# Kernel tuning notes

Measured on AMD Instinct MI355X. Metric: run time of the kernel, lower is better.

## Reference

```python
import jax, jax.numpy as jnp
import numpy as np

# neighbor-sampled node counts per hop level (outermost -> batch)
SIZES = (1363968, 123904, 11264, 1024)
E = (1239040, 112640, 10240)
D_IN, D_H, D_OUT = 128, 256, 64


def _sage(x_src, x_dst, src, dst, Wl, bl, Wr):
    """PyG SAGEConv(aggr='mean') on bipartite (x_src, x_dst) graph."""
    n_dst = x_dst.shape[0]
    agg = jax.ops.segment_sum(x_src[src], dst, num_segments=n_dst)
    cnt = jax.ops.segment_sum(jnp.ones((src.shape[0],), x_src.dtype), dst, num_segments=n_dst)
    mean = agg / jnp.maximum(cnt, 1.0)[:, None]
    return mean @ Wl + bl + x_dst @ Wr  # lin_l(mean) + lin_r(x_dst), lin_r has no bias


def setup_inputs() -> dict:
    key = jax.random.key(0)
    ks = jax.random.split(key, 16)
    inp = {}
    inp["x"] = jax.random.normal(ks[0], (SIZES[0], D_IN), dtype=jnp.float32)
    dims = [(D_IN, D_H), (D_H, D_H), (D_H, D_OUT)]
    for i, (di, do) in enumerate(dims):
        s = 1.0 / np.sqrt(di)
        inp[f"Wl{i}"] = jax.random.uniform(ks[1 + 3 * i], (di, do), jnp.float32, -s, s)
        inp[f"bl{i}"] = jax.random.uniform(ks[2 + 3 * i], (do,), jnp.float32, -s, s)
        inp[f"Wr{i}"] = jax.random.uniform(ks[3 + 3 * i], (di, do), jnp.float32, -s, s)
    for i in range(3):
        inp[f"edge_src{i}"] = jax.random.randint(ks[10 + i * 2], (E[i],), 0, SIZES[i], dtype=jnp.int32)
        inp[f"edge_dst{i}"] = jax.random.randint(ks[11 + i * 2 - 1], (E[i],), 0, SIZES[i + 1], dtype=jnp.int32)
    return inp


def reference(x, Wl0, bl0, Wr0, Wl1, bl1, Wr1, Wl2, bl2, Wr2,
              edge_src0, edge_dst0, edge_src1, edge_dst1, edge_src2, edge_dst2):
    # layer 0 (i=0 != num_layers-1=1 -> relu; dropout is identity in eval)
    h = _sage(x, x[:SIZES[1]], edge_src0, edge_dst0, Wl0, bl0, Wr0)
    h = jax.nn.relu(h)
    # layer 1 (i=1 == num_layers-1 -> no relu)
    h = _sage(h, h[:SIZES[2]], edge_src1, edge_dst1, Wl1, bl1, Wr1)
    # layer 2 (i=2 != 1 -> relu, faithful to the original quirk)
    h = _sage(h, h[:SIZES[3]], edge_src2, edge_dst2, Wl2, bl2, Wr2)
    h = jax.nn.relu(h)
    return h
```

## Files before the change

kernel.cpp:

```cpp
#include <hip/hip_runtime.h>

#define SZ0 1363968
#define SZ1 123904
#define SZ2 11264
#define SZ3 1024
#define NE0 1239040
#define NE1 112640
#define NE2 10240
#define DIN 128
#define DH  256
#define DOUT 64

__global__ __launch_bounds__(256) void edge_hist(
    const int* __restrict__ dst, int* __restrict__ bk, int E)
{
    int e = blockIdx.x * 256 + threadIdx.x;
    if (e < E) atomicAdd(&bk[dst[e]], 1);
}

__global__ __launch_bounds__(1024) void scan_inplace(int* __restrict__ a, int n)
{
    __shared__ int sums[1024];
    const int t = threadIdx.x;
    const int C = (n + 1023) >> 10;
    const int lo = t * C;
    const int hi = min(lo + C, n);
    int s = 0;
    for (int i = lo; i < hi; i++) s += a[i];
    sums[t] = s;
    __syncthreads();
    for (int off = 1; off < 1024; off <<= 1) {
        int v = (t >= off) ? sums[t - off] : 0;
        __syncthreads();
        sums[t] += v;
        __syncthreads();
    }
    int pre = (t == 0) ? 0 : sums[t - 1];
    for (int i = lo; i < hi; i++) { int v = a[i]; a[i] = pre; pre += v; }
}

__global__ __launch_bounds__(256) void edge_bucket(
    const int* __restrict__ src, const int* __restrict__ dst,
    int* __restrict__ bk, int* __restrict__ perm, int E)
{
    int e = blockIdx.x * 256 + threadIdx.x;
    if (e < E) {
        int pos = atomicAdd(&bk[dst[e]], 1);
        perm[pos] = src[e];
    }
}

template <int D>
__global__ __launch_bounds__(256) void gather_mean(
    const float* __restrict__ X, const int* __restrict__ perm,
    const int* __restrict__ ends, float* __restrict__ out)
{
    constexpr int VEC = D / 64;
    const int wave = (blockIdx.x * 256 + threadIdx.x) >> 6;
    const int lane = threadIdx.x & 63;
    const int start = (wave == 0) ? 0 : ends[wave - 1];
    const int end = ends[wave];

    float acc0[VEC], acc1[VEC];
#pragma unroll
    for (int i = 0; i < VEC; i++) { acc0[i] = 0.0f; acc1[i] = 0.0f; }

    int e = start;
    for (; e + 2 <= end; e += 2) {
        int s0 = perm[e];
        int s1 = perm[e + 1];
        const float* p0 = X + (size_t)s0 * D + lane * VEC;
        const float* p1 = X + (size_t)s1 * D + lane * VEC;
        if (VEC == 2) {
            float2 v0 = *reinterpret_cast<const float2*>(p0);
            float2 v1 = *reinterpret_cast<const float2*>(p1);
            acc0[0] += v0.x; acc0[1] += v0.y;
            acc1[0] += v1.x; acc1[1] += v1.y;
        } else {
            float4 v0 = *reinterpret_cast<const float4*>(p0);
            float4 v1 = *reinterpret_cast<const float4*>(p1);
            acc0[0] += v0.x; acc0[1] += v0.y; acc0[2] += v0.z; acc0[3] += v0.w;
            acc1[0] += v1.x; acc1[1] += v1.y; acc1[2] += v1.z; acc1[3] += v1.w;
        }
    }
    if (e < end) {
        int s0 = perm[e];
        const float* p0 = X + (size_t)s0 * D + lane * VEC;
        if (VEC == 2) {
            float2 v0 = *reinterpret_cast<const float2*>(p0);
            acc0[0] += v0.x; acc0[1] += v0.y;
        } else {
            float4 v0 = *reinterpret_cast<const float4*>(p0);
            acc0[0] += v0.x; acc0[1] += v0.y; acc0[2] += v0.z; acc0[3] += v0.w;
        }
    }

    const float inv = 1.0f / (float)max(end - start, 1);
    float* o = out + (size_t)wave * D + lane * VEC;
    if (VEC == 2) {
        float2 v;
        v.x = (acc0[0] + acc1[0]) * inv;
        v.y = (acc0[1] + acc1[1]) * inv;
        *reinterpret_cast<float2*>(o) = v;
    } else {
        float4 v;
        v.x = (acc0[0] + acc1[0]) * inv;
        v.y = (acc0[1] + acc1[1]) * inv;
        v.z = (acc0[2] + acc1[2]) * inv;
        v.w = (acc0[3] + acc1[3]) * inv;
        *reinterpret_cast<float4*>(o) = v;
    }
}

template <int BM, int BN>
__global__ __launch_bounds__(256) void gemm_sage(
    const float* __restrict__ A1, const float* __restrict__ A2,
    const float* __restrict__ B1, const float* __restrict__ B2,
    const float* __restrict__ bias, float* __restrict__ C,
    int K1, int K2, int do_relu)
{
    constexpr int BK = 32;
    constexpr int ROWS = BM / 16;
    constexpr int G = BN / 64;
    constexpr int AF4 = (BM * 8) / 256;
    constexpr int BF4 = (BN * 8) / 256;

    __shared__ float As[BK][BM + 4];
    __shared__ float Bs[BK][BN + 4];

    const int tid = threadIdx.x;
    const int m0 = blockIdx.x * BM;
    const int ty = tid >> 4;
    const int tx = tid & 15;

    float acc[ROWS][G * 4];
#pragma unroll
    for (int i = 0; i < ROWS; i++)
#pragma unroll
        for (int j = 0; j < G * 4; j++) acc[i][j] = 0.0f;

    const int K = K1 + K2;
    for (int kt = 0; kt < K; kt += BK) {
        const float* Ap; const float* Bp; int lK, kof;
        if (kt < K1) { Ap = A1; Bp = B1; lK = K1; kof = kt; }
        else         { Ap = A2; Bp = B2; lK = K2; kof = kt - K1; }

#pragma unroll
        for (int j = 0; j < AF4; j++) {
            int id = tid * AF4 + j;
            int m = id >> 3;
            int q = id & 7;
            float4 v = *reinterpret_cast<const float4*>(
                Ap + (size_t)(m0 + m) * lK + kof + q * 4);
            As[q * 4 + 0][m] = v.x;
            As[q * 4 + 1][m] = v.y;
            As[q * 4 + 2][m] = v.z;
            As[q * 4 + 3][m] = v.w;
        }
#pragma unroll
        for (int j = 0; j < BF4; j++) {
            int id = tid * BF4 + j;
            int k = id / (BN / 4);
            int c = id % (BN / 4);
            float4 v = *reinterpret_cast<const float4*>(
                Bp + (size_t)(kof + k) * BN + c * 4);
            *reinterpret_cast<float4*>(&Bs[k][c * 4]) = v;
        }
        __syncthreads();

#pragma unroll
        for (int kk = 0; kk < BK; kk++) {
            float a[ROWS];
            if constexpr (ROWS == 4) {
                float4 av = *reinterpret_cast<const float4*>(&As[kk][ty * 4]);
                a[0] = av.x; a[1] = av.y; a[2] = av.z; a[3] = av.w;
            } else {
                float2 av = *reinterpret_cast<const float2*>(&As[kk][ty * 2]);
                a[0] = av.x; a[1] = av.y;
            }
#pragma unroll
            for (int g = 0; g < G; g++) {
                float4 bv = *reinterpret_cast<const float4*>(&Bs[kk][g * 64 + tx * 4]);
                const float b[4] = {bv.x, bv.y, bv.z, bv.w};
#pragma unroll
                for (int i = 0; i < ROWS; i++)
#pragma unroll
                    for (int jj = 0; jj < 4; jj++)
                        acc[i][g * 4 + jj] += a[i] * b[jj];
            }
        }
        __syncthreads();
    }

#pragma unroll
    for (int i = 0; i < ROWS; i++) {
        const int row = m0 + ty * ROWS + i;
#pragma unroll
        for (int g = 0; g < G; g++) {
            const float4 bb = *reinterpret_cast<const float4*>(bias + g * 64 + tx * 4);
            float v0 = acc[i][g * 4 + 0] + bb.x;
            float v1 = acc[i][g * 4 + 1] + bb.y;
            float v2 = acc[i][g * 4 + 2] + bb.z;
            float v3 = acc[i][g * 4 + 3] + bb.w;
            if (do_relu) {
                v0 = fmaxf(v0, 0.0f); v1 = fmaxf(v1, 0.0f);
                v2 = fmaxf(v2, 0.0f); v3 = fmaxf(v3, 0.0f);
            }
            float4 o; o.x = v0; o.y = v1; o.z = v2; o.w = v3;
            *reinterpret_cast<float4*>(C + (size_t)row * BN + g * 64 + tx * 4) = o;
        }
    }
}

extern "C" void kernel_launch(void* const* d_in, const int* in_sizes, int n_in,
                              void* d_out, int out_size, void* d_ws, size_t ws_size,
                              hipStream_t stream)
{
    const float* x   = (const float*)d_in[0];
    const float* Wl0 = (const float*)d_in[1];
    const float* bl0 = (const float*)d_in[2];
    const float* Wr0 = (const float*)d_in[3];
    const float* Wl1 = (const float*)d_in[4];
    const float* bl1 = (const float*)d_in[5];
    const float* Wr1 = (const float*)d_in[6];
    const float* Wl2 = (const float*)d_in[7];
    const float* bl2 = (const float*)d_in[8];
    const float* Wr2 = (const float*)d_in[9];
    const int* es0 = (const int*)d_in[10];
    const int* ed0 = (const int*)d_in[11];
    const int* es1 = (const int*)d_in[12];
    const int* ed1 = (const int*)d_in[13];
    const int* es2 = (const int*)d_in[14];
    const int* ed2 = (const int*)d_in[15];

    int* bk0   = (int*)d_ws;
    int* bk1   = bk0 + SZ1;
    int* bk2   = bk1 + SZ2;
    int* perm0 = bk2 + SZ3;
    int* perm1 = perm0 + NE0;
    int* perm2 = perm1 + NE1;
    float* agg0 = (float*)(perm2 + NE2);
    float* agg1 = agg0 + (size_t)SZ1 * DIN;
    float* agg2 = agg1 + (size_t)SZ2 * DH;
    float* h1   = agg2 + (size_t)SZ3 * DH;
    float* h2   = agg0;

    hipMemsetAsync(bk0, 0, (size_t)(SZ1 + SZ2 + SZ3) * sizeof(int), stream);

    edge_hist<<<(NE0 + 255) / 256, 256, 0, stream>>>(ed0, bk0, NE0);
    scan_inplace<<<1, 1024, 0, stream>>>(bk0, SZ1);
    edge_bucket<<<(NE0 + 255) / 256, 256, 0, stream>>>(es0, ed0, bk0, perm0, NE0);
    gather_mean<DIN><<<SZ1 / 4, 256, 0, stream>>>(x, perm0, bk0, agg0);
    gemm_sage<64, DH><<<SZ1 / 64, 256, 0, stream>>>(
        agg0, x, Wl0, Wr0, bl0, h1, DIN, DIN, 1);

    edge_hist<<<(NE1 + 255) / 256, 256, 0, stream>>>(ed1, bk1, NE1);
    scan_inplace<<<1, 1024, 0, stream>>>(bk1, SZ2);
    edge_bucket<<<(NE1 + 255) / 256, 256, 0, stream>>>(es1, ed1, bk1, perm1, NE1);
    gather_mean<DH><<<SZ2 / 4, 256, 0, stream>>>(h1, perm1, bk1, agg1);
    gemm_sage<32, DH><<<SZ2 / 32, 256, 0, stream>>>(
        agg1, h1, Wl1, Wr1, bl1, h2, DH, DH, 0);

    edge_hist<<<(NE2 + 255) / 256, 256, 0, stream>>>(ed2, bk2, NE2);
    scan_inplace<<<1, 1024, 0, stream>>>(bk2, SZ3);
    edge_bucket<<<(NE2 + 255) / 256, 256, 0, stream>>>(es2, ed2, bk2, perm2, NE2);
    gather_mean<DH><<<SZ3 / 4, 256, 0, stream>>>(h2, perm2, bk2, agg2);
    gemm_sage<32, DOUT><<<SZ3 / 32, 256, 0, stream>>>(
        agg2, h2, Wl2, Wr2, bl2, (float*)d_out, DH, DH, 1);
}
```

Measured before the change: 1.643 ms.

## Fuse layer-0 gather-mean into GEMM and batch CSR build across layers

Layer 0's neighbor mean aggregation is now computed directly into shared memory inside a fused gather+GEMM kernel. This removes the round trip of the 123904x128 aggregate buffer through global memory and one launch. The histogram, scan and bucket passes for all three layers are merged into single launches, cutting nine small kernels to three and letting the three scans run in parallel blocks. The gather_mean kernel is specialized to float4 only, and h2 gets its own buffer instead of aliasing agg0.

```diff
diff --git a/kernel.cpp b/kernel.cpp
--- a/kernel.cpp
+++ b/kernel.cpp
@@ -11,16 +11,31 @@
 #define DH  256
 #define DOUT 64
 
-__global__ __launch_bounds__(256) void edge_hist(
-    const int* __restrict__ dst, int* __restrict__ bk, int E)
+__global__ __launch_bounds__(256) void hist_all(
+    const int* __restrict__ ed0, const int* __restrict__ ed1,
+    const int* __restrict__ ed2, int* __restrict__ bk0,
+    int* __restrict__ bk1, int* __restrict__ bk2)
 {
     int e = blockIdx.x * 256 + threadIdx.x;
-    if (e < E) atomicAdd(&bk[dst[e]], 1);
-}
-
-__global__ __launch_bounds__(1024) void scan_inplace(int* __restrict__ a, int n)
+    if (e < NE0) {
+        atomicAdd(&bk0[ed0[e]], 1);
+    } else if (e < NE0 + NE1) {
+        atomicAdd(&bk1[ed1[e - NE0]], 1);
+    } else {
+        atomicAdd(&bk2[ed2[e - NE0 - NE1]], 1);
+    }
+}
+
+__global__ __launch_bounds__(1024) void scan_all(
+    int* __restrict__ a0, int n0, int* __restrict__ a1, int n1,
+    int* __restrict__ a2, int n2)
 {
     __shared__ int sums[1024];
+    int* a; int n;
+    if (blockIdx.x == 0)      { a = a0; n = n0; }
+    else if (blockIdx.x == 1) { a = a1; n = n1; }
+    else                      { a = a2; n = n2; }
+
     const int t = threadIdx.x;
     const int C = (n + 1023) >> 10;
     const int lo = t * C;
@@ -39,14 +54,25 @@
     for (int i = lo; i < hi; i++) { int v = a[i]; a[i] = pre; pre += v; }
 }
 
-__global__ __launch_bounds__(256) void edge_bucket(
-    const int* __restrict__ src, const int* __restrict__ dst,
-    int* __restrict__ bk, int* __restrict__ perm, int E)
+__global__ __launch_bounds__(256) void bucket_all(
+    const int* __restrict__ es0, const int* __restrict__ ed0,
+    const int* __restrict__ es1, const int* __restrict__ ed1,
+    const int* __restrict__ es2, const int* __restrict__ ed2,
+    int* __restrict__ bk0, int* __restrict__ bk1, int* __restrict__ bk2,
+    int* __restrict__ p0, int* __restrict__ p1, int* __restrict__ p2)
 {
     int e = blockIdx.x * 256 + threadIdx.x;
-    if (e < E) {
-        int pos = atomicAdd(&bk[dst[e]], 1);
-        perm[pos] = src[e];
+    if (e < NE0) {
+        int pos = atomicAdd(&bk0[ed0[e]], 1);
+        p0[pos] = es0[e];
+    } else if (e < NE0 + NE1) {
+        int i = e - NE0;
+        int pos = atomicAdd(&bk1[ed1[i]], 1);
+        p1[pos] = es1[i];
+    } else {
+        int i = e - NE0 - NE1;
+        int pos = atomicAdd(&bk2[ed2[i]], 1);
+        p2[pos] = es2[i];
     }
 }
 
@@ -71,44 +97,140 @@
         int s1 = perm[e + 1];
         const float* p0 = X + (size_t)s0 * D + lane * VEC;
         const float* p1 = X + (size_t)s1 * D + lane * VEC;
-        if (VEC == 2) {
-            float2 v0 = *reinterpret_cast<const float2*>(p0);
-            float2 v1 = *reinterpret_cast<const float2*>(p1);
-            acc0[0] += v0.x; acc0[1] += v0.y;
-            acc1[0] += v1.x; acc1[1] += v1.y;
-        } else {
-            float4 v0 = *reinterpret_cast<const float4*>(p0);
-            float4 v1 = *reinterpret_cast<const float4*>(p1);
-            acc0[0] += v0.x; acc0[1] += v0.y; acc0[2] += v0.z; acc0[3] += v0.w;
-            acc1[0] += v1.x; acc1[1] += v1.y; acc1[2] += v1.z; acc1[3] += v1.w;
-        }
+        float4 v0 = *reinterpret_cast<const float4*>(p0);
+        float4 v1 = *reinterpret_cast<const float4*>(p1);
+        acc0[0] += v0.x; acc0[1] += v0.y; acc0[2] += v0.z; acc0[3] += v0.w;
+        acc1[0] += v1.x; acc1[1] += v1.y; acc1[2] += v1.z; acc1[3] += v1.w;
     }
     if (e < end) {
         int s0 = perm[e];
         const float* p0 = X + (size_t)s0 * D + lane * VEC;
-        if (VEC == 2) {
-            float2 v0 = *reinterpret_cast<const float2*>(p0);
-            acc0[0] += v0.x; acc0[1] += v0.y;
-        } else {
-            float4 v0 = *reinterpret_cast<const float4*>(p0);
-            acc0[0] += v0.x; acc0[1] += v0.y; acc0[2] += v0.z; acc0[3] += v0.w;
-        }
+        float4 v0 = *reinterpret_cast<const float4*>(p0);
+        acc0[0] += v0.x; acc0[1] += v0.y; acc0[2] += v0.z; acc0[3] += v0.w;
     }
 
     const float inv = 1.0f / (float)max(end - start, 1);
     float* o = out + (size_t)wave * D + lane * VEC;
-    if (VEC == 2) {
-        float2 v;
-        v.x = (acc0[0] + acc1[0]) * inv;
-        v.y = (acc0[1] + acc1[1]) * inv;
-        *reinterpret_cast<float2*>(o) = v;
-    } else {
-        float4 v;
-        v.x = (acc0[0] + acc1[0]) * inv;
-        v.y = (acc0[1] + acc1[1]) * inv;
-        v.z = (acc0[2] + acc1[2]) * inv;
-        v.w = (acc0[3] + acc1[3]) * inv;
-        *reinterpret_cast<float4*>(o) = v;
+    float4 v;
+    v.x = (acc0[0] + acc1[0]) * inv;
+    v.y = (acc0[1] + acc1[1]) * inv;
+    v.z = (acc0[2] + acc1[2]) * inv;
+    v.w = (acc0[3] + acc1[3]) * inv;
+    *reinterpret_cast<float4*>(o) = v;
+}
+
+__global__ __launch_bounds__(256) void fused_sage0(
+    const float* __restrict__ X, const int* __restrict__ perm,
+    const int* __restrict__ ends, const float* __restrict__ B1,
+    const float* __restrict__ B2, const float* __restrict__ bias,
+    float* __restrict__ C)
+{
+    __shared__ float Am[DIN][68];
+    __shared__ float Bs[32][260];
+
+    const int tid = threadIdx.x;
+    const int m0 = blockIdx.x * 64;
+    const int wv = tid >> 6;
+    const int lane = tid & 63;
+
+    for (int r = wv; r < 64; r += 4) {
+        const int row = m0 + r;
+        const int start = (row == 0) ? 0 : ends[row - 1];
+        const int end = ends[row];
+        float a0 = 0, a1 = 0, b0 = 0, b1 = 0, c0 = 0, c1 = 0, d0 = 0, d1 = 0;
+        int e = start;
+        for (; e + 4 <= end; e += 4) {
+            int s0 = perm[e], s1 = perm[e + 1], s2 = perm[e + 2], s3 = perm[e + 3];
+            float2 v0 = *(const float2*)(X + (size_t)s0 * DIN + lane * 2);
+            float2 v1 = *(const float2*)(X + (size_t)s1 * DIN + lane * 2);
+            float2 v2 = *(const float2*)(X + (size_t)s2 * DIN + lane * 2);
+            float2 v3 = *(const float2*)(X + (size_t)s3 * DIN + lane * 2);
+            a0 += v0.x; a1 += v0.y; b0 += v1.x; b1 += v1.y;
+            c0 += v2.x; c1 += v2.y; d0 += v3.x; d1 += v3.y;
+        }
+        for (; e < end; e++) {
+            int s0 = perm[e];
+            float2 v0 = *(const float2*)(X + (size_t)s0 * DIN + lane * 2);
+            a0 += v0.x; a1 += v0.y;
+        }
+        const float inv = 1.0f / (float)max(end - start, 1);
+        Am[lane * 2 + 0][r] = (a0 + b0 + c0 + d0) * inv;
+        Am[lane * 2 + 1][r] = (a1 + b1 + c1 + d1) * inv;
+    }
+    __syncthreads();
+
+    const int ty = tid >> 4;
+    const int tx = tid & 15;
+
+    float acc[4][16];
+#pragma unroll
+    for (int i = 0; i < 4; i++)
+#pragma unroll
+        for (int j = 0; j < 16; j++) acc[i][j] = 0.0f;
+
+    for (int kt = 0; kt < 2 * DIN; kt += 32) {
+        int abase;
+        if (kt < DIN) {
+            abase = kt;
+        } else {
+            abase = 0;
+#pragma unroll
+            for (int j = 0; j < 2; j++) {
+                int id = tid * 2 + j;
+                int m = id >> 3;
+                int q = id & 7;
+                float4 v = *reinterpret_cast<const float4*>(
+                    X + (size_t)(m0 + m) * DIN + (kt - DIN) + q * 4);
+                Am[q * 4 + 0][m] = v.x;
+                Am[q * 4 + 1][m] = v.y;
+                Am[q * 4 + 2][m] = v.z;
+                Am[q * 4 + 3][m] = v.w;
+            }
+        }
+        const float* Bp = (kt < DIN) ? B1 : B2;
+        const int kof = (kt < DIN) ? kt : kt - DIN;
+#pragma unroll
+        for (int j = 0; j < 8; j++) {
+            int id = tid * 8 + j;
+            int k = id >> 6;
+            int c = id & 63;
+            float4 v = *reinterpret_cast<const float4*>(
+                Bp + (size_t)(kof + k) * DH + c * 4);
+            *reinterpret_cast<float4*>(&Bs[k][c * 4]) = v;
+        }
+        __syncthreads();
+
+#pragma unroll
+        for (int kk = 0; kk < 32; kk++) {
+            float4 av = *reinterpret_cast<const float4*>(&Am[abase + kk][ty * 4]);
+            const float a[4] = {av.x, av.y, av.z, av.w};
+#pragma unroll
+            for (int g = 0; g < 4; g++) {
+                float4 bv = *reinterpret_cast<const float4*>(&Bs[kk][g * 64 + tx * 4]);
+                const float b[4] = {bv.x, bv.y, bv.z, bv.w};
+#pragma unroll
+                for (int i = 0; i < 4; i++)
+#pragma unroll
+                    for (int jj = 0; jj < 4; jj++)
+                        acc[i][g * 4 + jj] += a[i] * b[jj];
+            }
+        }
+        __syncthreads();
+    }
+
+#pragma unroll
+    for (int i = 0; i < 4; i++) {
+        const int row = m0 + ty * 4 + i;
+#pragma unroll
+        for (int g = 0; g < 4; g++) {
+            const float4 bb = *reinterpret_cast<const float4*>(bias + g * 64 + tx * 4);
+            float v0 = fmaxf(acc[i][g * 4 + 0] + bb.x, 0.0f);
+            float v1 = fmaxf(acc[i][g * 4 + 1] + bb.y, 0.0f);
+            float v2 = fmaxf(acc[i][g * 4 + 2] + bb.z, 0.0f);
+            float v3 = fmaxf(acc[i][g * 4 + 3] + bb.w, 0.0f);
+            float4 o; o.x = v0; o.y = v1; o.z = v2; o.w = v3;
+            *reinterpret_cast<float4*>(C + (size_t)row * DH + g * 64 + tx * 4) = o;
+        }
     }
 }
 
@@ -239,31 +361,25 @@
     int* perm0 = bk2 + SZ3;
     int* perm1 = perm0 + NE0;
     int* perm2 = perm1 + NE1;
-    float* agg0 = (float*)(perm2 + NE2);
-    float* agg1 = agg0 + (size_t)SZ1 * DIN;
+    float* agg1 = (float*)(perm2 + NE2);
     float* agg2 = agg1 + (size_t)SZ2 * DH;
     float* h1   = agg2 + (size_t)SZ3 * DH;
-    float* h2   = agg0;
+    float* h2   = h1 + (size_t)SZ1 * DH;
 
     hipMemsetAsync(bk0, 0, (size_t)(SZ1 + SZ2 + SZ3) * sizeof(int), stream);
 
-    edge_hist<<<(NE0 + 255) / 256, 256, 0, stream>>>(ed0, bk0, NE0);
-    scan_inplace<<<1, 1024, 0, stream>>>(bk0, SZ1);
-    edge_bucket<<<(NE0 + 255) / 256, 256, 0, stream>>>(es0, ed0, bk0, perm0, NE0);
-    gather_mean<DIN><<<SZ1 / 4, 256, 0, stream>>>(x, perm0, bk0, agg0);
-    gemm_sage<64, DH><<<SZ1 / 64, 256, 0, stream>>>(
-        agg0, x, Wl0, Wr0, bl0, h1, DIN, DIN, 1);
-
-    edge_hist<<<(NE1 + 255) / 256, 256, 0, stream>>>(ed1, bk1, NE1);
-    scan_inplace<<<1, 1024, 0, stream>>>(bk1, SZ2);
-    edge_bucket<<<(NE1 + 255) / 256, 256, 0, stream>>>(es1, ed1, bk1, perm1, NE1);
+    constexpr int NET = NE0 + NE1 + NE2;
+    hist_all<<<NET / 256, 256, 0, stream>>>(ed0, ed1, ed2, bk0, bk1, bk2);
+    scan_all<<<3, 1024, 0, stream>>>(bk0, SZ1, bk1, SZ2, bk2, SZ3);
+    bucket_all<<<NET / 256, 256, 0, stream>>>(es0, ed0, es1, ed1, es2, ed2,
+                                              bk0, bk1, bk2, perm0, perm1, perm2);
+
+    fused_sage0<<<SZ1 / 64, 256, 0, stream>>>(x, perm0, bk0, Wl0, Wr0, bl0, h1);
+
     gather_mean<DH><<<SZ2 / 4, 256, 0, stream>>>(h1, perm1, bk1, agg1);
     gemm_sage<32, DH><<<SZ2 / 32, 256, 0, stream>>>(
         agg1, h1, Wl1, Wr1, bl1, h2, DH, DH, 0);
 
-    edge_hist<<<(NE2 + 255) / 256, 256, 0, stream>>>(ed2, bk2, NE2);
-    scan_inplace<<<1, 1024, 0, stream>>>(bk2, SZ3);
-    edge_bucket<<<(NE2 + 255) / 256, 256, 0, stream>>>(es2, ed2, bk2, perm2, NE2);
     gather_mean<DH><<<SZ3 / 4, 256, 0, stream>>>(h2, perm2, bk2, agg2);
     gemm_sage<32, DOUT><<<SZ3 / 32, 256, 0, stream>>>(
         agg2, h2, Wl2, Wr2, bl2, (float*)d_out, DH, DH, 1);
```

Result: slower. 1.751 ms (+6.6%).

## Batch edge bucketing for all layers into three launches; unroll gather by four

Applied to the files above, without the earlier changes.

Merges the per-layer histogram, scan and bucket kernels into single launches that cover all three hop levels, with blockIdx selecting which layer each scan block handles. This cuts six kernel launches and lets the three small layers' preprocessing run alongside layer 0 instead of serially between compute stages. Separately, the mean-gather loop now keeps four independent accumulators and issues four row loads per iteration to raise memory-level parallelism. NET is divisible by 256, so the grid has no bounds issue; the costs are extra registers and a different float summation order.

```diff
diff --git a/kernel.cpp b/kernel.cpp
--- a/kernel.cpp
+++ b/kernel.cpp
@@ -11,16 +11,31 @@
 #define DH  256
 #define DOUT 64
 
-__global__ __launch_bounds__(256) void edge_hist(
-    const int* __restrict__ dst, int* __restrict__ bk, int E)
+__global__ __launch_bounds__(256) void hist_all(
+    const int* __restrict__ ed0, const int* __restrict__ ed1,
+    const int* __restrict__ ed2, int* __restrict__ bk0,
+    int* __restrict__ bk1, int* __restrict__ bk2)
 {
     int e = blockIdx.x * 256 + threadIdx.x;
-    if (e < E) atomicAdd(&bk[dst[e]], 1);
-}
-
-__global__ __launch_bounds__(1024) void scan_inplace(int* __restrict__ a, int n)
+    if (e < NE0) {
+        atomicAdd(&bk0[ed0[e]], 1);
+    } else if (e < NE0 + NE1) {
+        atomicAdd(&bk1[ed1[e - NE0]], 1);
+    } else {
+        atomicAdd(&bk2[ed2[e - NE0 - NE1]], 1);
+    }
+}
+
+__global__ __launch_bounds__(1024) void scan_all(
+    int* __restrict__ a0, int n0, int* __restrict__ a1, int n1,
+    int* __restrict__ a2, int n2)
 {
     __shared__ int sums[1024];
+    int* a; int n;
+    if (blockIdx.x == 0)      { a = a0; n = n0; }
+    else if (blockIdx.x == 1) { a = a1; n = n1; }
+    else                      { a = a2; n = n2; }
+
     const int t = threadIdx.x;
     const int C = (n + 1023) >> 10;
     const int lo = t * C;
@@ -39,14 +54,25 @@
     for (int i = lo; i < hi; i++) { int v = a[i]; a[i] = pre; pre += v; }
 }
 
-__global__ __launch_bounds__(256) void edge_bucket(
-    const int* __restrict__ src, const int* __restrict__ dst,
-    int* __restrict__ bk, int* __restrict__ perm, int E)
+__global__ __launch_bounds__(256) void bucket_all(
+    const int* __restrict__ es0, const int* __restrict__ ed0,
+    const int* __restrict__ es1, const int* __restrict__ ed1,
+    const int* __restrict__ es2, const int* __restrict__ ed2,
+    int* __restrict__ bk0, int* __restrict__ bk1, int* __restrict__ bk2,
+    int* __restrict__ p0, int* __restrict__ p1, int* __restrict__ p2)
 {
     int e = blockIdx.x * 256 + threadIdx.x;
-    if (e < E) {
-        int pos = atomicAdd(&bk[dst[e]], 1);
-        perm[pos] = src[e];
+    if (e < NE0) {
+        int pos = atomicAdd(&bk0[ed0[e]], 1);
+        p0[pos] = es0[e];
+    } else if (e < NE0 + NE1) {
+        int i = e - NE0;
+        int pos = atomicAdd(&bk1[ed1[i]], 1);
+        p1[pos] = es1[i];
+    } else {
+        int i = e - NE0 - NE1;
+        int pos = atomicAdd(&bk2[ed2[i]], 1);
+        p2[pos] = es2[i];
     }
 }
 
@@ -61,37 +87,48 @@
     const int start = (wave == 0) ? 0 : ends[wave - 1];
     const int end = ends[wave];
 
-    float acc0[VEC], acc1[VEC];
-#pragma unroll
-    for (int i = 0; i < VEC; i++) { acc0[i] = 0.0f; acc1[i] = 0.0f; }
+    float acc[4][VEC];
+#pragma unroll
+    for (int u = 0; u < 4; u++)
+#pragma unroll
+        for (int i = 0; i < VEC; i++) acc[u][i] = 0.0f;
 
     int e = start;
-    for (; e + 2 <= end; e += 2) {
-        int s0 = perm[e];
-        int s1 = perm[e + 1];
+    for (; e + 4 <= end; e += 4) {
+        int s0 = perm[e], s1 = perm[e + 1], s2 = perm[e + 2], s3 = perm[e + 3];
         const float* p0 = X + (size_t)s0 * D + lane * VEC;
         const float* p1 = X + (size_t)s1 * D + lane * VEC;
+        const float* p2 = X + (size_t)s2 * D + lane * VEC;
+        const float* p3 = X + (size_t)s3 * D + lane * VEC;
         if (VEC == 2) {
             float2 v0 = *reinterpret_cast<const float2*>(p0);
             float2 v1 = *reinterpret_cast<const float2*>(p1);
-            acc0[0] += v0.x; acc0[1] += v0.y;
-            acc1[0] += v1.x; acc1[1] += v1.y;
+            float2 v2 = *reinterpret_cast<const float2*>(p2);
+            float2 v3 = *reinterpret_cast<const float2*>(p3);
+            acc[0][0] += v0.x; acc[0][1] += v0.y;
+            acc[1][0] += v1.x; acc[1][1] += v1.y;
+            acc[2][0] += v2.x; acc[2][1] += v2.y;
+            acc[3][0] += v3.x; acc[3][1] += v3.y;
         } else {
             float4 v0 = *reinterpret_cast<const float4*>(p0);
             float4 v1 = *reinterpret_cast<const float4*>(p1);
-            acc0[0] += v0.x; acc0[1] += v0.y; acc0[2] += v0.z; acc0[3] += v0.w;
-            acc1[0] += v1.x; acc1[1] += v1.y; acc1[2] += v1.z; acc1[3] += v1.w;
-        }
-    }
-    if (e < end) {
+            float4 v2 = *reinterpret_cast<const float4*>(p2);
+            float4 v3 = *reinterpret_cast<const float4*>(p3);
+            acc[0][0] += v0.x; acc[0][1] += v0.y; acc[0][2] += v0.z; acc[0][3] += v0.w;
+            acc[1][0] += v1.x; acc[1][1] += v1.y; acc[1][2] += v1.z; acc[1][3] += v1.w;
+            acc[2][0] += v2.x; acc[2][1] += v2.y; acc[2][2] += v2.z; acc[2][3] += v2.w;
+            acc[3][0] += v3.x; acc[3][1] += v3.y; acc[3][2] += v3.z; acc[3][3] += v3.w;
+        }
+    }
+    for (; e < end; e++) {
         int s0 = perm[e];
         const float* p0 = X + (size_t)s0 * D + lane * VEC;
         if (VEC == 2) {
             float2 v0 = *reinterpret_cast<const float2*>(p0);
-            acc0[0] += v0.x; acc0[1] += v0.y;
+            acc[0][0] += v0.x; acc[0][1] += v0.y;
         } else {
             float4 v0 = *reinterpret_cast<const float4*>(p0);
-            acc0[0] += v0.x; acc0[1] += v0.y; acc0[2] += v0.z; acc0[3] += v0.w;
+            acc[0][0] += v0.x; acc[0][1] += v0.y; acc[0][2] += v0.z; acc[0][3] += v0.w;
         }
     }
 
@@ -99,15 +136,15 @@
     float* o = out + (size_t)wave * D + lane * VEC;
     if (VEC == 2) {
         float2 v;
-        v.x = (acc0[0] + acc1[0]) * inv;
-        v.y = (acc0[1] + acc1[1]) * inv;
+        v.x = (acc[0][0] + acc[1][0] + acc[2][0] + acc[3][0]) * inv;
+        v.y = (acc[0][1] + acc[1][1] + acc[2][1] + acc[3][1]) * inv;
         *reinterpret_cast<float2*>(o) = v;
     } else {
         float4 v;
-        v.x = (acc0[0] + acc1[0]) * inv;
-        v.y = (acc0[1] + acc1[1]) * inv;
-        v.z = (acc0[2] + acc1[2]) * inv;
-        v.w = (acc0[3] + acc1[3]) * inv;
+        v.x = (acc[0][0] + acc[1][0] + acc[2][0] + acc[3][0]) * inv;
+        v.y = (acc[0][1] + acc[1][1] + acc[2][1] + acc[3][1]) * inv;
+        v.z = (acc[0][2] + acc[1][2] + acc[2][2] + acc[3][2]) * inv;
+        v.w = (acc[0][3] + acc[1][3] + acc[2][3] + acc[3][3]) * inv;
         *reinterpret_cast<float4*>(o) = v;
     }
 }
@@ -247,23 +284,20 @@
 
     hipMemsetAsync(bk0, 0, (size_t)(SZ1 + SZ2 + SZ3) * sizeof(int), stream);
 
-    edge_hist<<<(NE0 + 255) / 256, 256, 0, stream>>>(ed0, bk0, NE0);
-    scan_inplace<<<1, 1024, 0, stream>>>(bk0, SZ1);
-    edge_bucket<<<(NE0 + 255) / 256, 256, 0, stream>>>(es0, ed0, bk0, perm0, NE0);
+    constexpr int NET = NE0 + NE1 + NE2;
+    hist_all<<<NET / 256, 256, 0, stream>>>(ed0, ed1, ed2, bk0, bk1, bk2);
+    scan_all<<<3, 1024, 0, stream>>>(bk0, SZ1, bk1, SZ2, bk2, SZ3);
+    bucket_all<<<NET / 256, 256, 0, stream>>>(es0, ed0, es1, ed1, es2, ed2,
+                                              bk0, bk1, bk2, perm0, perm1, perm2);
+
     gather_mean<DIN><<<SZ1 / 4, 256, 0, stream>>>(x, perm0, bk0, agg0);
     gemm_sage<64, DH><<<SZ1 / 64, 256, 0, stream>>>(
         agg0, x, Wl0, Wr0, bl0, h1, DIN, DIN, 1);
 
-    edge_hist<<<(NE1 + 255) / 256, 256, 0, stream>>>(ed1, bk1, NE1);
-    scan_inplace<<<1, 1024, 0, stream>>>(bk1, SZ2);
-    edge_bucket<<<(NE1 + 255) / 256, 256, 0, stream>>>(es1, ed1, bk1, perm1, NE1);
     gather_mean<DH><<<SZ2 / 4, 256, 0, stream>>>(h1, perm1, bk1, agg1);
     gemm_sage<32, DH><<<SZ2 / 32, 256, 0, stream>>>(
         agg1, h1, Wl1, Wr1, bl1, h2, DH, DH, 0);
 
-    edge_hist<<<(NE2 + 255) / 256, 256, 0, stream>>>(ed2, bk2, NE2);
-    scan_inplace<<<1, 1024, 0, stream>>>(bk2, SZ3);
-    edge_bucket<<<(NE2 + 255) / 256, 256, 0, stream>>>(es2, ed2, bk2, perm2, NE2);
     gather_mean<DH><<<SZ3 / 4, 256, 0, stream>>>(h2, perm2, bk2, agg2);
     gemm_sage<32, DOUT><<<SZ3 / 32, 256, 0, stream>>>(
         agg2, h2, Wl2, Wr2, bl2, (float*)d_out, DH, DH, 1);
```

Result: faster. 1.608 ms (-2.1%).
